# Optimization experiments

Hardware: AMD Instinct MI355X
Metric: run time of the kernel (lower is better)

The kernel has to match this reference:

```python
import jax, jax.numpy as jnp
import numpy as np

N_NODES = 100000
N_EDGES = 1600000
IN_FEATS = 128
HIDDEN = 128
OUT_DIM = 128


def setup_inputs() -> dict:
    key = jax.random.key(0)
    ks = jax.random.split(key, 8)
    x = jax.random.normal(ks[0], (N_NODES, IN_FEATS), dtype=jnp.float32)
    W1 = jax.random.normal(ks[1], (IN_FEATS, HIDDEN), dtype=jnp.float32) * (1.0 / np.sqrt(IN_FEATS))
    b1 = jnp.zeros((HIDDEN,), dtype=jnp.float32)
    W2 = jax.random.normal(ks[2], (HIDDEN, HIDDEN), dtype=jnp.float32) * (1.0 / np.sqrt(HIDDEN))
    b2 = jnp.zeros((HIDDEN,), dtype=jnp.float32)
    W3 = jax.random.normal(ks[3], (HIDDEN, OUT_DIM), dtype=jnp.float32) * (1.0 / np.sqrt(HIDDEN))
    b3 = jnp.zeros((OUT_DIM,), dtype=jnp.float32)
    edge_src = jax.random.randint(ks[4], (N_EDGES,), 0, N_NODES, dtype=jnp.int32)
    edge_dst = jax.random.randint(ks[5], (N_EDGES,), 0, N_NODES, dtype=jnp.int32)
    return {"x": x, "W1": W1, "b1": b1, "W2": W2, "b2": b2, "W3": W3, "b3": b3,
            "edge_src": edge_src, "edge_dst": edge_dst}


def _mean_agg(h, edge_src, edge_dst, inv_deg):
    # gather src features, scatter-sum to dst, divide by in-degree (mean)
    summed = jax.ops.segment_sum(h[edge_src], edge_dst, num_segments=N_NODES)
    return summed * inv_deg[:, None]


def reference(x, W1, b1, W2, b2, W3, b3, edge_src, edge_dst):
    # in-degree (clamped to 1 to avoid div-by-zero, matching mean over empty = 0)
    deg = jax.ops.segment_sum(jnp.ones((N_EDGES,), dtype=jnp.float32), edge_dst,
                              num_segments=N_NODES)
    inv_deg = 1.0 / jnp.maximum(deg, 1.0)

    # DGL GINConv (eps=0, mean): h = Linear(h + mean_neighbors(h))
    h = x
    h = (h + _mean_agg(h, edge_src, edge_dst, inv_deg)) @ W1 + b1
    h = jax.nn.relu(h)  # dropout inactive in eval mode
    h = (h + _mean_agg(h, edge_src, edge_dst, inv_deg)) @ W2 + b2
    h = jax.nn.relu(h)
    h = (h + _mean_agg(h, edge_src, edge_dst, inv_deg)) @ W3 + b3
    return h
```

## Files before the change

### kernel.cpp

```cpp
#include <hip/hip_runtime.h>
#include <hip/hip_bf16.h>
#include <stdint.h>

#if __has_builtin(__builtin_amdgcn_cvt_pk_f32_fp8) && __has_builtin(__builtin_amdgcn_cvt_pk_fp8_f32)
#define FP8_HW 1
#else
#define FP8_HW 0
#include <hip/hip_fp8.h>
#endif

#define N_NODES 100000
#define N_EDGES 1600000
#define FEAT 128

#define BKT_SHIFT 8
#define BKT_SIZE  256
#define NB_BKT    391
#define BKT_CAP   5120
#define NB_SC     800
#define EPB_SC    2000

typedef uint16_t u16;
typedef uint32_t u32;
typedef __attribute__((ext_vector_type(8))) short bf16x8;
typedef __attribute__((ext_vector_type(4))) float f32x4;
typedef __attribute__((ext_vector_type(2))) float f32x2;

__device__ __forceinline__ u16 bf16_rn(float f){
  u32 u = __float_as_uint(f);
  u += 0x7FFFu + ((u >> 16) & 1u);
  return (u16)(u >> 16);
}
__device__ __forceinline__ float bf16_lo(u32 p){ return __uint_as_float(p << 16); }
__device__ __forceinline__ float bf16_hi(u32 p){ return __uint_as_float(p & 0xFFFF0000u); }

__device__ __forceinline__ void fp8x4_to_f32(u32 w, float* o){
#if FP8_HW
  f32x2 a = __builtin_amdgcn_cvt_pk_f32_fp8(w, false);
  f32x2 b = __builtin_amdgcn_cvt_pk_f32_fp8(w, true);
  o[0] = a.x; o[1] = a.y; o[2] = b.x; o[3] = b.y;
#else
  #pragma unroll
  for (int i = 0; i < 4; ++i){
    __hip_fp8_e4m3 t; t.__x = (uint8_t)((w >> (8 * i)) & 0xFF);
    o[i] = (float)t;
  }
#endif
}
__device__ __forceinline__ u32 f32x4_to_fp8(float a, float b, float c, float d){
#if FP8_HW
  u32 r = __builtin_amdgcn_cvt_pk_fp8_f32(a, b, 0, false);
  r = __builtin_amdgcn_cvt_pk_fp8_f32(c, d, r, true);
  return r;
#else
  __hip_fp8_e4m3 qa(a), qb(b), qc(c), qd(d);
  return (u32)qa.__x | ((u32)qb.__x << 8) | ((u32)qc.__x << 16) | ((u32)qd.__x << 24);
#endif
}


__global__ __launch_bounds__(512) void hist_kernel(const int* __restrict__ dst,
                                                   int* __restrict__ hcnt){
  __shared__ int h[NB_BKT];
  for (int i = threadIdx.x; i < NB_BKT; i += 512) h[i] = 0;
  __syncthreads();
  int base = blockIdx.x * EPB_SC;
  for (int e = base + threadIdx.x; e < base + EPB_SC; e += 512)
    atomicAdd(&h[dst[e] >> BKT_SHIFT], 1);
  __syncthreads();
  for (int i = threadIdx.x; i < NB_BKT; i += 512)
    hcnt[blockIdx.x * NB_BKT + i] = h[i];
}

__global__ void hscan_kernel(int* __restrict__ hcnt, int* __restrict__ cursor){
  __shared__ int s[256];
  int b = blockIdx.x, t = threadIdx.x;
  int v[4]; int sum = 0;
  #pragma unroll
  for (int j = 0; j < 4; ++j){
    int blk = 4 * t + j;
    v[j] = (blk < NB_SC) ? hcnt[blk * NB_BKT + b] : 0;
    sum += v[j];
  }
  s[t] = sum;
  __syncthreads();
  for (int d = 1; d < 256; d <<= 1){
    int add = (t >= d) ? s[t - d] : 0;
    __syncthreads();
    s[t] += add;
    __syncthreads();
  }
  int excl = s[t] - sum;
  #pragma unroll
  for (int j = 0; j < 4; ++j){
    int blk = 4 * t + j;
    if (blk < NB_SC){ hcnt[blk * NB_BKT + b] = excl; excl += v[j]; }
  }
  if (t == 255) cursor[b] = s[255];
}

__global__ __launch_bounds__(512) void scatter_kernel(const int* __restrict__ src,
                                                      const int* __restrict__ dst,
                                                      const int* __restrict__ hcnt,
                                                      uint2* __restrict__ bbuf){
  __shared__ int cur[NB_BKT];
  for (int i = threadIdx.x; i < NB_BKT; i += 512)
    cur[i] = hcnt[blockIdx.x * NB_BKT + i];
  __syncthreads();
  int base = blockIdx.x * EPB_SC;
  for (int e = base + threadIdx.x; e < base + EPB_SC; e += 512){
    int d = dst[e];
    int b = d >> BKT_SHIFT;
    int p = atomicAdd(&cur[b], 1);
    bbuf[(size_t)b * BKT_CAP + p] = make_uint2((u32)src[e], (u32)(d & (BKT_SIZE - 1)));
  }
}

__global__ __launch_bounds__(1024) void csr_build_kernel(const uint2* __restrict__ bbuf,
                                 const int* __restrict__ cursor,
                                 int* __restrict__ offs, int* __restrict__ deg,
                                 float* __restrict__ inv_deg, int* __restrict__ eidx){
  __shared__ int hist[BKT_SIZE];
  __shared__ int s[BKT_SIZE];
  __shared__ int cu[BKT_SIZE];
  int b = blockIdx.x;
  int t = threadIdx.x;
  int lo = b * BKT_CAP;
  int hi = lo + cursor[b];
  if (t < BKT_SIZE) hist[t] = 0;
  __syncthreads();
  for (int e = lo + t; e < hi; e += 1024)
    atomicAdd(&hist[bbuf[e].y], 1);
  __syncthreads();
  int v = 0, pv = 0;
  if (t < BKT_SIZE){
    v  = hist[t];
    pv = (v + 3) & ~3;
    s[t] = pv;
  }
  __syncthreads();
  for (int d = 1; d < BKT_SIZE; d <<= 1){
    int add = (t < BKT_SIZE && t >= d) ? s[t - d] : 0;
    __syncthreads();
    if (t < BKT_SIZE && t >= d) s[t] += add;
    __syncthreads();
  }
  if (t < BKT_SIZE){
    int excl = s[t] - pv;
    int node = b * BKT_SIZE + t;
    if (node < N_NODES){
      offs[node]    = lo + excl;
      deg[node]     = v;
      inv_deg[node] = 1.0f / fmaxf((float)v, 1.0f);
    }
    s[t]  = excl;
    cu[t] = 0;
  }
  __syncthreads();
  for (int e = lo + t; e < hi; e += 1024){
    uint2 q = bbuf[e];
    int p = atomicAdd(&cu[q.y], 1);
    eidx[lo + s[q.y] + p] = (int)q.x;
  }
}


__global__ void cvt_x8_kernel(const float* __restrict__ x, uint2* __restrict__ X8){
  int i = blockIdx.x * 256 + threadIdx.x;
  const float4* p = (const float4*)x + (size_t)i * 2;
  float4 a = p[0], b = p[1];
  uint2 o;
  o.x = f32x4_to_fp8(a.x, a.y, a.z, a.w);
  o.y = f32x4_to_fp8(b.x, b.y, b.z, b.w);
  X8[i] = o;
}

__global__ void wprep3_kernel(const float* __restrict__ W1, const float* __restrict__ W2,
                              const float* __restrict__ W3, u16* __restrict__ Wp1,
                              u16* __restrict__ Wp2, u16* __restrict__ Wp3){
  int which = blockIdx.x >> 6;
  int b     = blockIdx.x & 63;
  const float* W = (which == 0) ? W1 : (which == 1) ? W2 : W3;
  u16*        Wp = (which == 0) ? Wp1 : (which == 1) ? Wp2 : Wp3;
  int idx = b * 256 + threadIdx.x;
  int j    = idx & 7;
  int lane = (idx >> 3) & 63;
  int t    = idx >> 9;
  int k0 = t & 3, n0 = t >> 2;
  int k = k0 * 32 + (lane >> 4) * 8 + j;
  int n = n0 * 16 + (lane & 15);
  Wp[idx] = bf16_rn(W[k * FEAT + n]);
}


template<int SM, int OUT>
__global__ __launch_bounds__(512, 4) void layer_kernel(
    const u32* __restrict__ n8,
    const u16* __restrict__ hb,
    const float* __restrict__ xf,
    const int* __restrict__ offs,
    const int* __restrict__ deg,
    const float* __restrict__ inv_deg,
    const int* __restrict__ eidx,
    const u16* __restrict__ Wp,
    const float* __restrict__ bias,
    u16* __restrict__ Hout,
    u32* __restrict__ H8out,
    float* __restrict__ Fout){
  __shared__ u16 Tt[128 * FEAT];
  const int tid   = threadIdx.x;
  const int wid   = tid >> 6;
  const int lane  = tid & 63;
  const int nsub  = lane >> 4;
  const int slice = lane & 15;
  const int base  = blockIdx.x * 128;

  for (int g = 0; g < 4; ++g){
    int rrow  = wid * 16 + g * 4 + nsub;
    int node  = base + rrow;
    bool vn   = node < N_NODES;
    int nc    = vn ? node : 0;
    int start = offs[nc];
    int cnt   = vn ? deg[nc] : 0;
    const int* ep = eidx + start;

    float acc[8];
    #pragma unroll
    for (int j = 0; j < 8; ++j) acc[j] = 0.f;

    uint4 q = (cnt > 0) ? *(const uint4*)ep : make_uint4(0, 0, 0, 0);

    for (int e = 0; e < cnt; e += 4){
      uint4 qn = *(const uint4*)(ep + e + 4);
      int i0 = (int)q.x, i1 = (int)q.y, i2 = (int)q.z, i3 = (int)q.w;
      float f0 = 1.f;
      float f1 = (e + 1 < cnt) ? 1.f : 0.f; if (e + 1 >= cnt) i1 = 0;
      float f2 = (e + 2 < cnt) ? 1.f : 0.f; if (e + 2 >= cnt) i2 = 0;
      float f3 = (e + 3 < cnt) ? 1.f : 0.f; if (e + 3 >= cnt) i3 = 0;
      uint2 r0 = *(const uint2*)(n8 + (size_t)i0 * 32 + slice * 2);
      uint2 r1 = *(const uint2*)(n8 + (size_t)i1 * 32 + slice * 2);
      uint2 r2 = *(const uint2*)(n8 + (size_t)i2 * 32 + slice * 2);
      uint2 r3 = *(const uint2*)(n8 + (size_t)i3 * 32 + slice * 2);
      float t0[4], t1[4];
      fp8x4_to_f32(r0.x, t0); fp8x4_to_f32(r0.y, t1);
      acc[0]+=f0*t0[0]; acc[1]+=f0*t0[1]; acc[2]+=f0*t0[2]; acc[3]+=f0*t0[3];
      acc[4]+=f0*t1[0]; acc[5]+=f0*t1[1]; acc[6]+=f0*t1[2]; acc[7]+=f0*t1[3];
      fp8x4_to_f32(r1.x, t0); fp8x4_to_f32(r1.y, t1);
      acc[0]+=f1*t0[0]; acc[1]+=f1*t0[1]; acc[2]+=f1*t0[2]; acc[3]+=f1*t0[3];
      acc[4]+=f1*t1[0]; acc[5]+=f1*t1[1]; acc[6]+=f1*t1[2]; acc[7]+=f1*t1[3];
      fp8x4_to_f32(r2.x, t0); fp8x4_to_f32(r2.y, t1);
      acc[0]+=f2*t0[0]; acc[1]+=f2*t0[1]; acc[2]+=f2*t0[2]; acc[3]+=f2*t0[3];
      acc[4]+=f2*t1[0]; acc[5]+=f2*t1[1]; acc[6]+=f2*t1[2]; acc[7]+=f2*t1[3];
      fp8x4_to_f32(r3.x, t0); fp8x4_to_f32(r3.y, t1);
      acc[0]+=f3*t0[0]; acc[1]+=f3*t0[1]; acc[2]+=f3*t0[2]; acc[3]+=f3*t0[3];
      acc[4]+=f3*t1[0]; acc[5]+=f3*t1[1]; acc[6]+=f3*t1[2]; acc[7]+=f3*t1[3];
      q = qn;
    }

    uint4 o = make_uint4(0, 0, 0, 0);
    if (vn){
      float w = inv_deg[node];
      float self[8];
      if (SM == 1){
        const float* sp = xf + (size_t)node * FEAT + slice * 8;
        float4 a = *(const float4*)sp;
        float4 b = *(const float4*)(sp + 4);
        self[0]=a.x; self[1]=a.y; self[2]=a.z; self[3]=a.w;
        self[4]=b.x; self[5]=b.y; self[6]=b.z; self[7]=b.w;
      } else {
        const u16* sp = hb + (size_t)node * FEAT + slice * 8;
        uint4 s0 = *(const uint4*)sp;
        self[0]=bf16_lo(s0.x); self[1]=bf16_hi(s0.x); self[2]=bf16_lo(s0.y); self[3]=bf16_hi(s0.y);
        self[4]=bf16_lo(s0.z); self[5]=bf16_hi(s0.z); self[6]=bf16_lo(s0.w); self[7]=bf16_hi(s0.w);
      }
      o.x = (u32)bf16_rn(self[0] + w*acc[0]) | ((u32)bf16_rn(self[1] + w*acc[1]) << 16);
      o.y = (u32)bf16_rn(self[2] + w*acc[2]) | ((u32)bf16_rn(self[3] + w*acc[3]) << 16);
      o.z = (u32)bf16_rn(self[4] + w*acc[4]) | ((u32)bf16_rn(self[5] + w*acc[5]) << 16);
      o.w = (u32)bf16_rn(self[6] + w*acc[6]) | ((u32)bf16_rn(self[7] + w*acc[7]) << 16);
    }
    ((uint4*)Tt)[rrow * 16 + (slice ^ (rrow & 7))] = o;
  }
  __syncthreads();

  const int quad = lane >> 4;
  const int c    = lane & 15;
  const int r0   = wid * 16;

  bf16x8 A[4];
  #pragma unroll
  for (int k0 = 0; k0 < 4; ++k0){
    uint4 t = ((const uint4*)Tt)[(r0 + c) * 16 + ((quad + k0 * 4) ^ ((r0 + c) & 7))];
    A[k0] = *(const bf16x8*)&t;
  }

  f32x4 acc2[8];
  #pragma unroll
  for (int i = 0; i < 8; ++i) acc2[i] = (f32x4){0.f, 0.f, 0.f, 0.f};

  #pragma unroll
  for (int n0 = 0; n0 < 8; ++n0){
    #pragma unroll
    for (int k0 = 0; k0 < 4; ++k0){
      bf16x8 b = *(const bf16x8*)(Wp + (size_t)(((n0 << 2) | k0) * 64 + lane) * 8);
      acc2[n0] = __builtin_amdgcn_mfma_f32_16x16x32_bf16(A[k0], b, acc2[n0], 0, 0, 0);
    }
  }

  if (OUT == 1){
    #pragma unroll
    for (int n0 = 0; n0 < 8; ++n0){
      float bv = bias[n0 * 16 + c];
      #pragma unroll
      for (int r = 0; r < 4; ++r){
        int row = base + r0 + quad * 4 + r;
        if (row < N_NODES)
          Fout[(size_t)row * FEAT + n0 * 16 + c] = acc2[n0][r] + bv;
      }
    }
  } else {
    __syncthreads();
    #pragma unroll
    for (int n0 = 0; n0 < 8; ++n0){
      float bv = bias[n0 * 16 + c];
      #pragma unroll
      for (int r = 0; r < 4; ++r){
        int rr  = r0 + quad * 4 + r;
        int col = n0 * 16 + c;
        float v = fmaxf(acc2[n0][r] + bv, 0.f);
        Tt[rr * FEAT + (col ^ ((rr & 7) << 3))] = bf16_rn(v);
      }
    }
    __syncthreads();
    #pragma unroll
    for (int it = 0; it < 4; ++it){
      int p  = it * 512 + tid;
      int rr = p >> 4, qq = p & 15;
      int node = base + rr;
      if (node < N_NODES){
        uint4 d = ((const uint4*)Tt)[rr * 16 + (qq ^ (rr & 7))];
        *(uint4*)(Hout + (size_t)node * FEAT + qq * 8) = d;
        uint2 o8;
        o8.x = f32x4_to_fp8(bf16_lo(d.x), bf16_hi(d.x), bf16_lo(d.y), bf16_hi(d.y));
        o8.y = f32x4_to_fp8(bf16_lo(d.z), bf16_hi(d.z), bf16_lo(d.w), bf16_hi(d.w));
        *(uint2*)(H8out + (size_t)node * 32 + qq * 2) = o8;
      }
    }
  }
}


static inline size_t align_up(size_t x){ return (x + 255) & ~(size_t)255; }

extern "C" void kernel_launch(void* const* d_in, const int* in_sizes, int n_in,
                              void* d_out, int out_size, void* d_ws, size_t ws_size,
                              hipStream_t stream){
  const float* x  = (const float*)d_in[0];
  const float* W1 = (const float*)d_in[1];
  const float* b1 = (const float*)d_in[2];
  const float* W2 = (const float*)d_in[3];
  const float* b2 = (const float*)d_in[4];
  const float* W3 = (const float*)d_in[5];
  const float* b3 = (const float*)d_in[6];
  const int* esrc = (const int*)d_in[7];
  const int* edst = (const int*)d_in[8];

  char* w = (char*)d_ws;
  int*   cursor  = (int*)w;    w += align_up((size_t)NB_BKT * 4);
  int*   hcnt    = (int*)w;    w += align_up((size_t)NB_SC * NB_BKT * 4);
  int*   deg     = (int*)w;    w += align_up((size_t)N_NODES * 4);
  int*   offs    = (int*)w;    w += align_up((size_t)N_NODES * 4);
  float* inv_deg = (float*)w;  w += align_up((size_t)N_NODES * 4);
  int*   eidx    = (int*)w;    w += align_up((size_t)NB_BKT * BKT_CAP * 4);
  u16*   Wp1     = (u16*)w;    w += align_up((size_t)16384 * 2);
  u16*   Wp2     = (u16*)w;    w += align_up((size_t)16384 * 2);
  u16*   Wp3     = (u16*)w;    w += align_up((size_t)16384 * 2);
  u16*   Hb      = (u16*)w;    w += align_up((size_t)N_NODES * FEAT * 2);
  u32*   H8b     = (u32*)w;    w += align_up((size_t)N_NODES * 32 * 4);

  uint2* bbuf = (uint2*)Hb;

  u16* Ha  = (u16*)d_out;
  u32* H8a = (u32*)((char*)d_out + (size_t)N_NODES * FEAT * 2);
  u32* X8  = (u32*)((char*)d_out + (size_t)N_NODES * FEAT * 3);

  hist_kernel<<<NB_SC, 512, 0, stream>>>(edst, hcnt);
  hscan_kernel<<<NB_BKT, 256, 0, stream>>>(hcnt, cursor);
  scatter_kernel<<<NB_SC, 512, 0, stream>>>(esrc, edst, hcnt, bbuf);
  csr_build_kernel<<<NB_BKT, 1024, 0, stream>>>(bbuf, cursor, offs, deg, inv_deg, eidx);

  wprep3_kernel<<<192, 256, 0, stream>>>(W1, W2, W3, Wp1, Wp2, Wp3);
  cvt_x8_kernel<<<N_EDGES / 256, 256, 0, stream>>>(x, (uint2*)X8);

  const int LAYER_BLOCKS = (N_NODES + 127) / 128;

  layer_kernel<1, 0><<<LAYER_BLOCKS, 512, 0, stream>>>(
      X8, (const u16*)nullptr, x, offs, deg, inv_deg, eidx, Wp1, b1,
      Ha, H8a, (float*)nullptr);

  layer_kernel<0, 0><<<LAYER_BLOCKS, 512, 0, stream>>>(
      H8a, Ha, (const float*)nullptr, offs, deg, inv_deg, eidx, Wp2, b2,
      Hb, H8b, (float*)nullptr);

  layer_kernel<0, 1><<<LAYER_BLOCKS, 512, 0, stream>>>(
      H8b, Hb, (const float*)nullptr, offs, deg, inv_deg, eidx, Wp3, b3,
      (u16*)nullptr, (u32*)nullptr, (float*)d_out);

  (void)in_sizes; (void)n_in; (void)out_size; (void)ws_size; (void)w;
}
```

Measured before the change: 339.9 us.

## Use single-wave 16-node blocks with 8-edge padded gather loop

Layer kernels now run as one 64-thread wavefront per block handling 16 nodes, with a small shared tile, instead of 512-thread blocks over 128 nodes. This removes block-wide barriers and should let the scheduler balance irregular per-node degrees. The CSR build pads each node's edge list to a multiple of 8 with index 0. The gather loop then runs unpredicated 8-way with more loads in flight, and subtracts node 0's contribution once per padding slot afterward. The edge bucket capacity grows to hold the padding, and the temporary histogram buffers are aliased into an intermediate buffer. The risks are a larger edge array, the extra correction step, and less reuse of weight loads per block.

```diff
diff --git a/kernel.cpp b/kernel.cpp
--- a/kernel.cpp
+++ b/kernel.cpp
@@ -16,7 +16,7 @@
 #define BKT_SHIFT 8
 #define BKT_SIZE  256
 #define NB_BKT    391
-#define BKT_CAP   5120
+#define BKT_CAP   5664
 #define NB_SC     800
 #define EPB_SC    2000
 
@@ -135,7 +135,7 @@
   int v = 0, pv = 0;
   if (t < BKT_SIZE){
     v  = hist[t];
-    pv = (v + 3) & ~3;
+    pv = (v + 7) & ~7;
     s[t] = pv;
   }
   __syncthreads();
@@ -152,6 +152,7 @@
       offs[node]    = lo + excl;
       deg[node]     = v;
       inv_deg[node] = 1.0f / fmaxf((float)v, 1.0f);
+      for (int p = v; p < pv; ++p) eidx[lo + excl + p] = 0;
     }
     s[t]  = excl;
     cu[t] = 0;
@@ -194,7 +195,7 @@
 
 
 template<int SM, int OUT>
-__global__ __launch_bounds__(512, 4) void layer_kernel(
+__global__ __launch_bounds__(64, 8) void layer_kernel(
     const u32* __restrict__ n8,
     const u16* __restrict__ hb,
     const float* __restrict__ xf,
@@ -207,143 +208,136 @@
     u16* __restrict__ Hout,
     u32* __restrict__ H8out,
     float* __restrict__ Fout){
-  __shared__ u16 Tt[128 * FEAT];
+  __shared__ u16 Tt[16 * FEAT];
   const int tid   = threadIdx.x;
-  const int wid   = tid >> 6;
-  const int lane  = tid & 63;
-  const int nsub  = lane >> 4;
-  const int slice = lane & 15;
-  const int base  = blockIdx.x * 128;
+  const int nsub  = tid >> 4;
+  const int slice = tid & 15;
+  const int base  = blockIdx.x * 16;
 
   for (int g = 0; g < 4; ++g){
-    int rrow  = wid * 16 + g * 4 + nsub;
-    int node  = base + rrow;
-    bool vn   = node < N_NODES;
-    int nc    = vn ? node : 0;
-    int start = offs[nc];
-    int cnt   = vn ? deg[nc] : 0;
+    const int rrow = (g << 2) + nsub;
+    const int node = base + rrow;
+    const int start = offs[node];
+    const int cnt   = deg[node];
     const int* ep = eidx + start;
+    const int pcnt = (cnt + 7) & ~7;
 
     float acc[8];
     #pragma unroll
     for (int j = 0; j < 8; ++j) acc[j] = 0.f;
 
-    uint4 q = (cnt > 0) ? *(const uint4*)ep : make_uint4(0, 0, 0, 0);
-
-    for (int e = 0; e < cnt; e += 4){
-      uint4 qn = *(const uint4*)(ep + e + 4);
-      int i0 = (int)q.x, i1 = (int)q.y, i2 = (int)q.z, i3 = (int)q.w;
-      float f0 = 1.f;
-      float f1 = (e + 1 < cnt) ? 1.f : 0.f; if (e + 1 >= cnt) i1 = 0;
-      float f2 = (e + 2 < cnt) ? 1.f : 0.f; if (e + 2 >= cnt) i2 = 0;
-      float f3 = (e + 3 < cnt) ? 1.f : 0.f; if (e + 3 >= cnt) i3 = 0;
-      uint2 r0 = *(const uint2*)(n8 + (size_t)i0 * 32 + slice * 2);
-      uint2 r1 = *(const uint2*)(n8 + (size_t)i1 * 32 + slice * 2);
-      uint2 r2 = *(const uint2*)(n8 + (size_t)i2 * 32 + slice * 2);
-      uint2 r3 = *(const uint2*)(n8 + (size_t)i3 * 32 + slice * 2);
+    uint4 qa = make_uint4(0,0,0,0), qb = qa;
+    if (pcnt > 0){ qa = *(const uint4*)ep; qb = *(const uint4*)(ep + 4); }
+
+    for (int e = 0; e < pcnt; e += 8){
+      uint4 qa2 = *(const uint4*)(ep + e + 8);
+      uint4 qb2 = *(const uint4*)(ep + e + 12);
+      uint2 r0 = *(const uint2*)(n8 + (size_t)qa.x * 32 + slice * 2);
+      uint2 r1 = *(const uint2*)(n8 + (size_t)qa.y * 32 + slice * 2);
+      uint2 r2 = *(const uint2*)(n8 + (size_t)qa.z * 32 + slice * 2);
+      uint2 r3 = *(const uint2*)(n8 + (size_t)qa.w * 32 + slice * 2);
+      uint2 r4 = *(const uint2*)(n8 + (size_t)qb.x * 32 + slice * 2);
+      uint2 r5 = *(const uint2*)(n8 + (size_t)qb.y * 32 + slice * 2);
+      uint2 r6 = *(const uint2*)(n8 + (size_t)qb.z * 32 + slice * 2);
+      uint2 r7 = *(const uint2*)(n8 + (size_t)qb.w * 32 + slice * 2);
       float t0[4], t1[4];
-      fp8x4_to_f32(r0.x, t0); fp8x4_to_f32(r0.y, t1);
-      acc[0]+=f0*t0[0]; acc[1]+=f0*t0[1]; acc[2]+=f0*t0[2]; acc[3]+=f0*t0[3];
-      acc[4]+=f0*t1[0]; acc[5]+=f0*t1[1]; acc[6]+=f0*t1[2]; acc[7]+=f0*t1[3];
-      fp8x4_to_f32(r1.x, t0); fp8x4_to_f32(r1.y, t1);
-      acc[0]+=f1*t0[0]; acc[1]+=f1*t0[1]; acc[2]+=f1*t0[2]; acc[3]+=f1*t0[3];
-      acc[4]+=f1*t1[0]; acc[5]+=f1*t1[1]; acc[6]+=f1*t1[2]; acc[7]+=f1*t1[3];
-      fp8x4_to_f32(r2.x, t0); fp8x4_to_f32(r2.y, t1);
-      acc[0]+=f2*t0[0]; acc[1]+=f2*t0[1]; acc[2]+=f2*t0[2]; acc[3]+=f2*t0[3];
-      acc[4]+=f2*t1[0]; acc[5]+=f2*t1[1]; acc[6]+=f2*t1[2]; acc[7]+=f2*t1[3];
-      fp8x4_to_f32(r3.x, t0); fp8x4_to_f32(r3.y, t1);
-      acc[0]+=f3*t0[0]; acc[1]+=f3*t0[1]; acc[2]+=f3*t0[2]; acc[3]+=f3*t0[3];
-      acc[4]+=f3*t1[0]; acc[5]+=f3*t1[1]; acc[6]+=f3*t1[2]; acc[7]+=f3*t1[3];
-      q = qn;
-    }
-
-    uint4 o = make_uint4(0, 0, 0, 0);
-    if (vn){
-      float w = inv_deg[node];
-      float self[8];
-      if (SM == 1){
-        const float* sp = xf + (size_t)node * FEAT + slice * 8;
-        float4 a = *(const float4*)sp;
-        float4 b = *(const float4*)(sp + 4);
-        self[0]=a.x; self[1]=a.y; self[2]=a.z; self[3]=a.w;
-        self[4]=b.x; self[5]=b.y; self[6]=b.z; self[7]=b.w;
-      } else {
-        const u16* sp = hb + (size_t)node * FEAT + slice * 8;
-        uint4 s0 = *(const uint4*)sp;
-        self[0]=bf16_lo(s0.x); self[1]=bf16_hi(s0.x); self[2]=bf16_lo(s0.y); self[3]=bf16_hi(s0.y);
-        self[4]=bf16_lo(s0.z); self[5]=bf16_hi(s0.z); self[6]=bf16_lo(s0.w); self[7]=bf16_hi(s0.w);
-      }
-      o.x = (u32)bf16_rn(self[0] + w*acc[0]) | ((u32)bf16_rn(self[1] + w*acc[1]) << 16);
-      o.y = (u32)bf16_rn(self[2] + w*acc[2]) | ((u32)bf16_rn(self[3] + w*acc[3]) << 16);
-      o.z = (u32)bf16_rn(self[4] + w*acc[4]) | ((u32)bf16_rn(self[5] + w*acc[5]) << 16);
-      o.w = (u32)bf16_rn(self[6] + w*acc[6]) | ((u32)bf16_rn(self[7] + w*acc[7]) << 16);
-    }
+      #define ACC8(rr) \
+        fp8x4_to_f32(rr.x, t0); fp8x4_to_f32(rr.y, t1); \
+        acc[0]+=t0[0]; acc[1]+=t0[1]; acc[2]+=t0[2]; acc[3]+=t0[3]; \
+        acc[4]+=t1[0]; acc[5]+=t1[1]; acc[6]+=t1[2]; acc[7]+=t1[3];
+      ACC8(r0) ACC8(r1) ACC8(r2) ACC8(r3) ACC8(r4) ACC8(r5) ACC8(r6) ACC8(r7)
+      #undef ACC8
+      qa = qa2; qb = qb2;
+    }
+
+    if (pcnt > cnt){
+      float f = (float)(pcnt - cnt);
+      uint2 rz = *(const uint2*)(n8 + slice * 2);
+      float t0[4], t1[4];
+      fp8x4_to_f32(rz.x, t0); fp8x4_to_f32(rz.y, t1);
+      acc[0]-=f*t0[0]; acc[1]-=f*t0[1]; acc[2]-=f*t0[2]; acc[3]-=f*t0[3];
+      acc[4]-=f*t1[0]; acc[5]-=f*t1[1]; acc[6]-=f*t1[2]; acc[7]-=f*t1[3];
+    }
+
+    const float w = inv_deg[node];
+    float self[8];
+    if (SM == 1){
+      const float* sp = xf + (size_t)node * FEAT + slice * 8;
+      float4 a = *(const float4*)sp;
+      float4 b = *(const float4*)(sp + 4);
+      self[0]=a.x; self[1]=a.y; self[2]=a.z; self[3]=a.w;
+      self[4]=b.x; self[5]=b.y; self[6]=b.z; self[7]=b.w;
+    } else {
+      const u16* sp = hb + (size_t)node * FEAT + slice * 8;
+      uint4 s0 = *(const uint4*)sp;
+      self[0]=bf16_lo(s0.x); self[1]=bf16_hi(s0.x); self[2]=bf16_lo(s0.y); self[3]=bf16_hi(s0.y);
+      self[4]=bf16_lo(s0.z); self[5]=bf16_hi(s0.z); self[6]=bf16_lo(s0.w); self[7]=bf16_hi(s0.w);
+    }
+    uint4 o;
+    o.x = (u32)bf16_rn(self[0] + w*acc[0]) | ((u32)bf16_rn(self[1] + w*acc[1]) << 16);
+    o.y = (u32)bf16_rn(self[2] + w*acc[2]) | ((u32)bf16_rn(self[3] + w*acc[3]) << 16);
+    o.z = (u32)bf16_rn(self[4] + w*acc[4]) | ((u32)bf16_rn(self[5] + w*acc[5]) << 16);
+    o.w = (u32)bf16_rn(self[6] + w*acc[6]) | ((u32)bf16_rn(self[7] + w*acc[7]) << 16);
     ((uint4*)Tt)[rrow * 16 + (slice ^ (rrow & 7))] = o;
   }
   __syncthreads();
 
-  const int quad = lane >> 4;
-  const int c    = lane & 15;
-  const int r0   = wid * 16;
+  const int quad = tid >> 4;
+  const int c    = tid & 15;
 
   bf16x8 A[4];
   #pragma unroll
   for (int k0 = 0; k0 < 4; ++k0){
-    uint4 t = ((const uint4*)Tt)[(r0 + c) * 16 + ((quad + k0 * 4) ^ ((r0 + c) & 7))];
+    uint4 t = ((const uint4*)Tt)[c * 16 + ((quad + k0 * 4) ^ (c & 7))];
     A[k0] = *(const bf16x8*)&t;
   }
-
-  f32x4 acc2[8];
+  if (OUT == 0) __syncthreads();
+
   #pragma unroll
-  for (int i = 0; i < 8; ++i) acc2[i] = (f32x4){0.f, 0.f, 0.f, 0.f};
-
-  #pragma unroll
-  for (int n0 = 0; n0 < 8; ++n0){
+  for (int h = 0; h < 2; ++h){
+    f32x4 acc2[4];
     #pragma unroll
-    for (int k0 = 0; k0 < 4; ++k0){
-      bf16x8 b = *(const bf16x8*)(Wp + (size_t)(((n0 << 2) | k0) * 64 + lane) * 8);
-      acc2[n0] = __builtin_amdgcn_mfma_f32_16x16x32_bf16(A[k0], b, acc2[n0], 0, 0, 0);
-    }
-  }
-
-  if (OUT == 1){
+    for (int i = 0; i < 4; ++i) acc2[i] = (f32x4){0.f, 0.f, 0.f, 0.f};
     #pragma unroll
-    for (int n0 = 0; n0 < 8; ++n0){
+    for (int i = 0; i < 4; ++i){
+      int n0 = h * 4 + i;
+      #pragma unroll
+      for (int k0 = 0; k0 < 4; ++k0){
+        bf16x8 b = *(const bf16x8*)(Wp + (size_t)(((n0 << 2) | k0) * 64 + tid) * 8);
+        acc2[i] = __builtin_amdgcn_mfma_f32_16x16x32_bf16(A[k0], b, acc2[i], 0, 0, 0);
+      }
+    }
+    #pragma unroll
+    for (int i = 0; i < 4; ++i){
+      int n0 = h * 4 + i;
       float bv = bias[n0 * 16 + c];
       #pragma unroll
       for (int r = 0; r < 4; ++r){
-        int row = base + r0 + quad * 4 + r;
-        if (row < N_NODES)
-          Fout[(size_t)row * FEAT + n0 * 16 + c] = acc2[n0][r] + bv;
+        int rr  = quad * 4 + r;
+        int col = n0 * 16 + c;
+        if (OUT == 1){
+          Fout[(size_t)(base + rr) * FEAT + col] = acc2[i][r] + bv;
+        } else {
+          float v = fmaxf(acc2[i][r] + bv, 0.f);
+          Tt[rr * FEAT + (col ^ ((rr & 7) << 3))] = bf16_rn(v);
+        }
       }
     }
-  } else {
-    __syncthreads();
-    #pragma unroll
-    for (int n0 = 0; n0 < 8; ++n0){
-      float bv = bias[n0 * 16 + c];
-      #pragma unroll
-      for (int r = 0; r < 4; ++r){
-        int rr  = r0 + quad * 4 + r;
-        int col = n0 * 16 + c;
-        float v = fmaxf(acc2[n0][r] + bv, 0.f);
-        Tt[rr * FEAT + (col ^ ((rr & 7) << 3))] = bf16_rn(v);
-      }
-    }
+  }
+
+  if (OUT == 0){
     __syncthreads();
     #pragma unroll
     for (int it = 0; it < 4; ++it){
-      int p  = it * 512 + tid;
+      int p  = it * 64 + tid;
       int rr = p >> 4, qq = p & 15;
       int node = base + rr;
-      if (node < N_NODES){
-        uint4 d = ((const uint4*)Tt)[rr * 16 + (qq ^ (rr & 7))];
-        *(uint4*)(Hout + (size_t)node * FEAT + qq * 8) = d;
-        uint2 o8;
-        o8.x = f32x4_to_fp8(bf16_lo(d.x), bf16_hi(d.x), bf16_lo(d.y), bf16_hi(d.y));
-        o8.y = f32x4_to_fp8(bf16_lo(d.z), bf16_hi(d.z), bf16_lo(d.w), bf16_hi(d.w));
-        *(uint2*)(H8out + (size_t)node * 32 + qq * 2) = o8;
-      }
+      uint4 d = ((const uint4*)Tt)[rr * 16 + (qq ^ (rr & 7))];
+      *(uint4*)(Hout + (size_t)node * FEAT + qq * 8) = d;
+      uint2 o8;
+      o8.x = f32x4_to_fp8(bf16_lo(d.x), bf16_hi(d.x), bf16_lo(d.y), bf16_hi(d.y));
+      o8.y = f32x4_to_fp8(bf16_lo(d.z), bf16_hi(d.z), bf16_lo(d.w), bf16_hi(d.w));
+      *(uint2*)(H8out + (size_t)node * 32 + qq * 2) = o8;
     }
   }
 }
@@ -365,8 +359,6 @@
   const int* edst = (const int*)d_in[8];
 
   char* w = (char*)d_ws;
-  int*   cursor  = (int*)w;    w += align_up((size_t)NB_BKT * 4);
-  int*   hcnt    = (int*)w;    w += align_up((size_t)NB_SC * NB_BKT * 4);
   int*   deg     = (int*)w;    w += align_up((size_t)N_NODES * 4);
   int*   offs    = (int*)w;    w += align_up((size_t)N_NODES * 4);
   float* inv_deg = (float*)w;  w += align_up((size_t)N_NODES * 4);
@@ -377,7 +369,9 @@
   u16*   Hb      = (u16*)w;    w += align_up((size_t)N_NODES * FEAT * 2);
   u32*   H8b     = (u32*)w;    w += align_up((size_t)N_NODES * 32 * 4);
 
-  uint2* bbuf = (uint2*)Hb;
+  uint2* bbuf   = (uint2*)Hb;
+  int*   cursor = (int*)H8b;
+  int*   hcnt   = (int*)((char*)H8b + align_up((size_t)NB_BKT * 4));
 
   u16* Ha  = (u16*)d_out;
   u32* H8a = (u32*)((char*)d_out + (size_t)N_NODES * FEAT * 2);
@@ -391,17 +385,17 @@
   wprep3_kernel<<<192, 256, 0, stream>>>(W1, W2, W3, Wp1, Wp2, Wp3);
   cvt_x8_kernel<<<N_EDGES / 256, 256, 0, stream>>>(x, (uint2*)X8);
 
-  const int LAYER_BLOCKS = (N_NODES + 127) / 128;
-
-  layer_kernel<1, 0><<<LAYER_BLOCKS, 512, 0, stream>>>(
+  const int LAYER_BLOCKS = N_NODES / 16;
+
+  layer_kernel<1, 0><<<LAYER_BLOCKS, 64, 0, stream>>>(
       X8, (const u16*)nullptr, x, offs, deg, inv_deg, eidx, Wp1, b1,
       Ha, H8a, (float*)nullptr);
 
-  layer_kernel<0, 0><<<LAYER_BLOCKS, 512, 0, stream>>>(
+  layer_kernel<0, 0><<<LAYER_BLOCKS, 64, 0, stream>>>(
       H8a, Ha, (const float*)nullptr, offs, deg, inv_deg, eidx, Wp2, b2,
       Hb, H8b, (float*)nullptr);
 
-  layer_kernel<0, 1><<<LAYER_BLOCKS, 512, 0, stream>>>(
+  layer_kernel<0, 1><<<LAYER_BLOCKS, 64, 0, stream>>>(
       H8b, Hb, (const float*)nullptr, offs, deg, inv_deg, eidx, Wp3, b3,
       (u16*)nullptr, (u32*)nullptr, (float*)d_out);
 
```

After: 302.7 us. 1.12x faster.
